# Kernel optimization log

Hardware: AMD Instinct MI355X
Metric: run time of the kernel (lower is better)

## Reference

```python
import jax, jax.numpy as jnp
import numpy as np
import math

B, C, T0, Q0 = 2, 48, 250, 65
H = 192; KS = 4; HS = 1; NH = 4; E = 8; F = 65; DV = 12; HID2 = 384
EPS = 1e-5


def ln_clamp(x, g, b, axes, eps=EPS):
    # LayerNormalization4D / 4DCF: std = sqrt(clamp(var, eps))
    mu = x.mean(axis=axes, keepdims=True)
    var = x.var(axis=axes, keepdims=True)
    return (x - mu) / jnp.sqrt(jnp.maximum(var, eps)) * g + b


def torch_ln(x, g, b, eps=EPS):
    # torch.nn.LayerNorm over last dim: sqrt(var + eps)
    mu = x.mean(axis=-1, keepdims=True)
    var = x.var(axis=-1, keepdims=True)
    return (x - mu) / jnp.sqrt(var + eps) * g + b


def mha(x, in_w, in_b, out_w, out_b, nh):
    # torch.nn.MultiheadAttention, batch_first, self-attention
    N, L, Cm = x.shape
    qkv = x @ in_w.T + in_b
    q, k, v = jnp.split(qkv, 3, axis=-1)
    dh = Cm // nh
    hd = lambda t: t.reshape(N, L, nh, dh).transpose(0, 2, 1, 3)
    q, k, v = hd(q), hd(k), hd(v)
    att = jax.nn.softmax(jnp.einsum('nhld,nhmd->nhlm', q, k) / jnp.sqrt(jnp.float32(dh)), axis=-1)
    o = jnp.einsum('nhlm,nhmd->nhld', att, v).transpose(0, 2, 1, 3).reshape(N, L, Cm)
    return o @ out_w.T + out_b


def lstm_dir(x, wi, wh, bi, bh, reverse=False):
    # x: [N, L, D]; torch gate order i,f,g,o
    Hd = wh.shape[1]
    xs = jnp.swapaxes(x, 0, 1)
    if reverse:
        xs = xs[::-1]
    pre = jnp.einsum('lnd,gd->lng', xs, wi) + bi + bh  # [L,N,4H]

    def step(carry, p):
        hprev, cprev = carry
        gates = p + hprev @ wh.T
        i, f, g, o = jnp.split(gates, 4, axis=-1)
        c = jax.nn.sigmoid(f) * cprev + jax.nn.sigmoid(i) * jnp.tanh(g)
        hnew = jax.nn.sigmoid(o) * jnp.tanh(c)
        return (hnew, c), hnew

    h0 = jnp.zeros((x.shape[0], Hd), x.dtype)
    _, ys = jax.lax.scan(step, (h0, h0), pre)
    if reverse:
        ys = ys[::-1]
    return jnp.swapaxes(ys, 0, 1)


def bilstm(x, wif, whf, bif, bhf, wib, whb, bib, bhb):
    return jnp.concatenate([lstm_dir(x, wif, whf, bif, bhf, False),
                            lstm_dir(x, wib, whb, bib, bhb, True)], axis=-1)


def unfold1d(x, ks, hs):
    # x: [N, C, Q] -> [N, L, C*ks], channel-major like F.unfold
    N, Cc, Qq = x.shape
    L = (Qq - ks) // hs + 1
    cols = jnp.stack([x[:, :, k:k + (L - 1) * hs + 1:hs] for k in range(ks)], axis=-1)  # [N,C,L,ks]
    return cols.transpose(0, 2, 1, 3).reshape(N, L, Cc * ks)


def conv_transpose1d(x, w, b, stride):
    # x: [N, Cin, L], w: [Cin, Cout, ks] (torch ConvTranspose1d layout); overlap-add
    N, Ci, L = x.shape
    ks = w.shape[2]
    out_len = (L - 1) * stride + ks
    y = jnp.einsum('nil,iok->nolk', x, w)
    out = jnp.zeros((N, w.shape[1], out_len), x.dtype)
    for k in range(ks):
        out = out.at[:, :, k:k + (L - 1) * stride + 1:stride].add(y[..., k])
    return out + b[:, None]


def _forward(x, af_in_w, af_in_b, af_out_w, af_out_b, naf_g, naf_b, at_in_w, at_in_b, at_out_w, at_out_b, nat_g, nat_b, intra_ng, intra_nb, inter_ng, inter_nb, intra_wif, intra_whf, intra_bif, intra_bhf, intra_wib, intra_whb, intra_bib, intra_bhb, inter_wif, inter_whf, inter_bif, inter_bhf, inter_wib, inter_whb, inter_bib, inter_bhb, il_w, il_b, itl_w, itl_b, qw, qb, qa, qg, qbt, kw, kb, ka, kg, kbt, vw, vb, va, vg, vbt, pw, pb, pa, pg, pbt, fin_w, fin_b, fdw_w, fdw_b, fout_w, fout_b):
    Bb, Cc, old_T, old_Q = x.shape
    T = math.ceil((old_T - KS) / HS) * HS + KS
    Qd = math.ceil((old_Q - KS) / HS) * HS + KS
    x = jnp.pad(x, ((0, 0), (0, 0), (0, T - old_T), (0, Qd - old_Q)))
    input_ = x

    # ---- intra (frequency) path ----
    z = ln_clamp(input_, intra_ng[None, :, None, None], intra_nb[None, :, None, None], (1,))
    seq = z.transpose(0, 2, 3, 1).reshape(Bb * T, Qd, Cc)  # [B*T, Q, C]
    att = mha(seq, af_in_w, af_in_b, af_out_w, af_out_b, NH)
    seq = torch_ln(att + seq, naf_g, naf_b)
    u = unfold1d(seq.transpose(0, 2, 1), KS, HS)
    r = bilstm(u, intra_wif, intra_whf, intra_bif, intra_bhf, intra_wib, intra_whb, intra_bib, intra_bhb)
    r = conv_transpose1d(r.transpose(0, 2, 1), il_w, il_b, HS)  # [B*T, C, Qd]
    intra = r.reshape(Bb, T, Cc, Qd).transpose(0, 2, 1, 3) + input_
    input_ = intra

    # ---- inter (time) path ----
    z = ln_clamp(input_, inter_ng[None, :, None, None], inter_nb[None, :, None, None], (1,))
    seq = z.transpose(0, 3, 2, 1).reshape(Bb * Qd, T, Cc)  # [B*Q, T, C]
    att = mha(seq, at_in_w, at_in_b, at_out_w, at_out_b, NH)
    seq = torch_ln(att + seq, nat_g, nat_b)
    u = unfold1d(seq.transpose(0, 2, 1), KS, HS)
    r = bilstm(u, inter_wif, inter_whf, inter_bif, inter_bhf, inter_wib, inter_whb, inter_bib, inter_bhb)
    r = conv_transpose1d(r.transpose(0, 2, 1), itl_w, itl_b, HS)  # [B*Qd, C, T]
    inter = r.reshape(Bb, Qd, Cc, T).transpose(0, 2, 3, 1) + input_
    inter = inter[:, :, :old_T, :old_Q]

    # ---- custom per-head conv attention ----
    bt = inter  # [B, C, t, f]

    def head_proj(w, bias, a, g, beta):
        y = jnp.einsum('bctf,hec->hbetf', bt, w) + bias[:, None, :, None, None]
        y = jnp.where(y >= 0, y, a[:, None, None, None, None] * y)  # PReLU per head
        return ln_clamp(y, g[:, None, :, None, :], beta[:, None, :, None, :], (2, 4))

    Qh = head_proj(qw, qb, qa, qg, qbt)  # [h,B,E,t,f]
    Kh = head_proj(kw, kb, ka, kg, kbt)
    Vh = head_proj(vw, vb, va, vg, vbt)  # [h,B,dv,t,f]
    h_, _, E_, t_, f_ = Qh.shape
    dv = Vh.shape[2]
    Qf = Qh.transpose(0, 1, 3, 2, 4).reshape(h_, Bb, t_, E_ * f_)
    Kf = Kh.transpose(0, 1, 3, 2, 4).reshape(h_, Bb, t_, E_ * f_)
    Vf = Vh.transpose(0, 1, 3, 2, 4).reshape(h_, Bb, t_, dv * f_)
    attm = jax.nn.softmax(jnp.einsum('hbtd,hbsd->hbts', Qf, Kf) / jnp.sqrt(jnp.float32(E_ * f_)), axis=-1)
    Vo = jnp.einsum('hbts,hbsd->hbtd', attm, Vf).reshape(h_, Bb, t_, dv, f_)
    Vo = Vo.transpose(1, 0, 3, 2, 4).reshape(Bb, h_ * dv, t_, f_)  # head-major channel concat
    pj = jnp.einsum('bctf,oc->botf', Vo, pw) + pb[None, :, None, None]
    pj = jnp.where(pj >= 0, pj, pa * pj)
    pj = ln_clamp(pj, pg[None, :, None, :], pbt[None, :, None, :], (1, 3))
    out = pj + inter

    # ---- gated-dconv FFN ----
    pi = jnp.einsum('bctf,oc->botf', out, fin_w) + fin_b[None, :, None, None]
    dwc = jax.lax.conv_general_dilated(pi, fdw_w, (1, 1), ((1, 1), (1, 1)),
                                       dimension_numbers=('NCHW', 'OIHW', 'NCHW'),
                                       feature_group_count=fdw_w.shape[0]) + fdw_b[None, :, None, None]
    x1, x2 = jnp.split(dwc, 2, axis=1)
    ffn = jnp.einsum('bctf,oc->botf', jax.nn.gelu(x1, approximate=False) * x2, fout_w) + fout_b[None, :, None, None]
    return ffn + out


def setup_inputs() -> dict:
    key = jax.random.key(0)
    cnt = [0]

    def rn(shape, s=0.05):
        cnt[0] += 1
        return jax.random.normal(jax.random.fold_in(key, cnt[0]), shape, dtype=jnp.float32) * s

    z = lambda *s: jnp.zeros(s, jnp.float32)
    o = lambda *s: jnp.ones(s, jnp.float32)
    d = {}
    d['x'] = rn((B, C, T0, Q0), 1.0)
    for p in ['af', 'at']:
        d[p + '_in_w'] = rn((3 * C, C)); d[p + '_in_b'] = z(3 * C)
        d[p + '_out_w'] = rn((C, C)); d[p + '_out_b'] = z(C)
    d['naf_g'] = o(C); d['naf_b'] = z(C); d['nat_g'] = o(C); d['nat_b'] = z(C)
    d['intra_ng'] = o(C); d['intra_nb'] = z(C); d['inter_ng'] = o(C); d['inter_nb'] = z(C)
    for p in ['intra', 'inter']:
        for s in ['f', 'b']:
            d[p + '_wi' + s] = rn((4 * H, C * KS)); d[p + '_wh' + s] = rn((4 * H, H))
            d[p + '_bi' + s] = z(4 * H); d[p + '_bh' + s] = z(4 * H)
    d['il_w'] = rn((2 * H, C, KS)); d['il_b'] = z(C)
    d['itl_w'] = rn((2 * H, C, KS)); d['itl_b'] = z(C)
    for p, dim in [('q', E), ('k', E), ('v', DV)]:
        d[p + 'w'] = rn((NH, dim, C)); d[p + 'b'] = z(NH, dim)
        d[p + 'a'] = 0.25 * o(NH); d[p + 'g'] = o(NH, dim, F); d[p + 'bt'] = z(NH, dim, F)
    d['pw'] = rn((C, C)); d['pb'] = z(C); d['pa'] = 0.25 * o(1); d['pg'] = o(C, F); d['pbt'] = z(C, F)
    d['fin_w'] = rn((HID2, C)); d['fin_b'] = z(HID2)
    d['fdw_w'] = rn((HID2, 1, 3, 3)); d['fdw_b'] = z(HID2)
    d['fout_w'] = rn((C, HID2 // 2)); d['fout_b'] = z(C)
    return d


def reference(x, af_in_w, af_in_b, af_out_w, af_out_b, naf_g, naf_b, at_in_w, at_in_b, at_out_w, at_out_b, nat_g, nat_b, intra_ng, intra_nb, inter_ng, inter_nb, intra_wif, intra_whf, intra_bif, intra_bhf, intra_wib, intra_whb, intra_bib, intra_bhb, inter_wif, inter_whf, inter_bif, inter_bhf, inter_wib, inter_whb, inter_bib, inter_bhb, il_w, il_b, itl_w, itl_b, qw, qb, qa, qg, qbt, kw, kb, ka, kg, kbt, vw, vb, va, vg, vbt, pw, pb, pa, pg, pbt, fin_w, fin_b, fdw_w, fdw_b, fout_w, fout_b):
    return _forward(x, af_in_w, af_in_b, af_out_w, af_out_b, naf_g, naf_b, at_in_w, at_in_b, at_out_w, at_out_b, nat_g, nat_b, intra_ng, intra_nb, inter_ng, inter_nb, intra_wif, intra_whf, intra_bif, intra_bhf, intra_wib, intra_whb, intra_bib, intra_bhb, inter_wif, inter_whf, inter_bif, inter_bhf, inter_wib, inter_whb, inter_bib, inter_bhb, il_w, il_b, itl_w, itl_b, qw, qb, qa, qg, qbt, kw, kb, ka, kg, kbt, vw, vb, va, vg, vbt, pw, pb, pa, pg, pbt, fin_w, fin_b, fdw_w, fdw_b, fout_w, fout_b)
```

## Files before the change

kernel.cpp:

```cpp
#include <hip/hip_runtime.h>
#include <math.h>

#define EPSV 1e-5f

typedef _Float16 v2h __attribute__((ext_vector_type(2)));

__device__ __forceinline__ float sigf(float x){ return 1.0f/(1.0f+__expf(-x)); }
__device__ __forceinline__ float tanhf_(float x){
  float c = fminf(fmaxf(x,-10.f),10.f);
  float e = __expf(2.0f*c);
  return (e-1.0f)/(e+1.0f);
}

__device__ __forceinline__ void ldsbar(){
  asm volatile("s_waitcnt lgkmcnt(0)\n\ts_barrier" ::: "memory");
}

__device__ __forceinline__ float dot2u(unsigned int a, unsigned int b, float c){
#if __has_builtin(__builtin_amdgcn_fdot2)
  v2h av = __builtin_bit_cast(v2h, a);
  v2h bv = __builtin_bit_cast(v2h, b);
  return __builtin_amdgcn_fdot2(av, bv, c, false);
#else
  v2h av = __builtin_bit_cast(v2h, a);
  v2h bv = __builtin_bit_cast(v2h, b);
  return c + (float)av.x*(float)bv.x + (float)av.y*(float)bv.y;
#endif
}

__global__ void k_ln_chan(const float* __restrict__ src, float* __restrict__ dst,
                          const float* __restrict__ g, const float* __restrict__ bb, int mode){
  int i = blockIdx.x*blockDim.x + threadIdx.x;
  const int total = 2*250*65;
  if (i >= total) return;
  int q = i % 65; int t = (i/65) % 250; int b = i/(65*250);
  const float* p = src + (size_t)b*48*250*65 + (size_t)t*65 + q;
  float s=0.f, ss=0.f;
  for (int c=0;c<48;c++){ float v = p[(size_t)c*250*65]; s+=v; ss+=v*v; }
  float mu = s*(1.0f/48.0f);
  float var = ss*(1.0f/48.0f) - mu*mu;
  float rs = rsqrtf(fmaxf(var, EPSV));
  float* d = (mode==0) ? dst + ((size_t)(b*250+t)*65 + q)*48
                       : dst + ((size_t)(b*65+q)*250 + t)*48;
  for (int c=0;c<48;c++){ float v = p[(size_t)c*250*65]; d[c] = (v-mu)*rs*g[c] + bb[c]; }
}

__global__ void k_qkv(const float* __restrict__ seq, const float* __restrict__ w,
                      const float* __restrict__ bias, float* __restrict__ qkv, int NL){
  int i = blockIdx.x*blockDim.x + threadIdx.x;
  if (i >= NL*144) return;
  int j = i % 144; int nl = i / 144;
  const float* srow = seq + (size_t)nl*48;
  const float* wrow = w + j*48;
  float acc = bias[j];
  for (int c=0;c<48;c++) acc += srow[c]*wrow[c];
  qkv[i] = acc;
}

__global__ void k_mha(const float* __restrict__ qkv, float* __restrict__ att, int N, int L){
  __shared__ float shq[250*12];
  __shared__ float shk[250*12];
  __shared__ float shv[250*12];
  int n = blockIdx.x, h = blockIdx.y;
  const float* base = qkv + (size_t)n*L*144 + h*12;
  for (int i = threadIdx.x; i < L*12; i += blockDim.x){
    int l = i/12, d = i%12;
    shq[i] = base[(size_t)l*144 + d];
    shk[i] = base[(size_t)l*144 + 48 + d];
    shv[i] = base[(size_t)l*144 + 96 + d];
  }
  __syncthreads();
  const float scale = 0.28867513459481287f;
  for (int r = threadIdx.x; r < L; r += blockDim.x){
    float m = -1e30f, den = 0.0f, o[12];
    for (int d=0; d<12; d++) o[d]=0.0f;
    const float* qr = shq + r*12;
    for (int j=0; j<L; j++){
      const float* kr = shk + j*12;
      float s = 0.f;
      for (int d=0; d<12; d++) s += qr[d]*kr[d];
      s *= scale;
      if (s > m){
        float corr = __expf(m - s);
        den *= corr;
        for (int d=0; d<12; d++) o[d] *= corr;
        m = s;
      }
      float e = __expf(s - m);
      den += e;
      const float* vr = shv + j*12;
      for (int d=0; d<12; d++) o[d] += e*vr[d];
    }
    float inv = 1.0f/den;
    float* outp = att + ((size_t)n*L + r)*48 + h*12;
    for (int d=0; d<12; d++) outp[d] = o[d]*inv;
  }
}

__global__ void k_projres(const float* __restrict__ att, const float* __restrict__ seq,
                          const float* __restrict__ w, const float* __restrict__ bias,
                          float* __restrict__ dst, int NL){
  int i = blockIdx.x*blockDim.x + threadIdx.x;
  if (i >= NL*48) return;
  int o = i % 48; int nl = i/48;
  const float* ar = att + (size_t)nl*48;
  const float* wr = w + o*48;
  float acc = bias[o] + seq[i];
  for (int c=0;c<48;c++) acc += ar[c]*wr[c];
  dst[i] = acc;
}

__global__ void k_rowln(float* __restrict__ buf, const float* __restrict__ g,
                        const float* __restrict__ bb, int NL){
  int nl = blockIdx.x*blockDim.x + threadIdx.x;
  if (nl >= NL) return;
  float* p = buf + (size_t)nl*48;
  float s=0.f, ss=0.f;
  for (int c=0;c<48;c++){ float v=p[c]; s+=v; ss+=v*v; }
  float mu = s*(1.0f/48.0f);
  float var = ss*(1.0f/48.0f) - mu*mu;
  float rs = rsqrtf(var + EPSV);
  for (int c=0;c<48;c++) p[c] = (p[c]-mu)*rs*g[c] + bb[c];
}

__global__ void k_prep(const float* __restrict__ s0, const float* __restrict__ s1,
                       const float* __restrict__ s2, const float* __restrict__ s3,
                       const float* __restrict__ s4, const float* __restrict__ s5,
                       const float* __restrict__ s6, const float* __restrict__ s7,
                       const float* __restrict__ c0, const float* __restrict__ c1,
                       unsigned int* __restrict__ wpk, unsigned int* __restrict__ wtp){
  int i = blockIdx.x*blockDim.x + threadIdx.x;
  if (i < 589824){
    int seg = i/73728, off = i - seg*73728;
    const float* w = (seg==0)?s0:(seg==1)?s1:(seg==2)?s2:(seg==3)?s3:(seg==4)?s4:(seg==5)?s5:(seg==6)?s6:s7;
    int g = off % 768, d2 = off / 768;
    v2h v; v.x = (_Float16)w[g*192 + 2*d2]; v.y = (_Float16)w[g*192 + 2*d2 + 1];
    wpk[(size_t)seg*73728 + (size_t)d2*768 + g] = __builtin_bit_cast(unsigned int, v);
  } else if (i < 589824 + 2*36864){
    int j = i - 589824;
    int seg = j/36864, off = j - seg*36864;
    const float* w = seg ? c1 : c0;
    int c = off % 48; int ii2 = (off/48) % 192; int k = off/(48*192);
    v2h v;
    v.x = (_Float16)w[(2*ii2)*192 + c*4 + k];
    v.y = (_Float16)w[(2*ii2+1)*192 + c*4 + k];
    wtp[(size_t)seg*36864 + off] = __builtin_bit_cast(unsigned int, v);
  }
}

__global__ __launch_bounds__(256) void k_pregates(
    const float* __restrict__ seq2, const unsigned int* __restrict__ wi,
    const float* __restrict__ bi, const float* __restrict__ bh,
    _Float16* __restrict__ pre, int L2, int SL){
  __shared__ unsigned int ut[96*16];
  int n = blockIdx.y;
  int l0 = blockIdx.x*16;
  int t = threadIdx.x;
  for (int idx=t; idx<1536; idx+=256){
    int l = idx & 15, d2 = idx >> 4;
    int li = l0 + l;
    int c = d2 >> 1, k0 = (d2 & 1)*2;
    float u0=0.f, u1=0.f;
    if (li < L2){
      const float* p = seq2 + ((size_t)n*SL + li)*48;
      u0 = p[k0*48 + c];
      u1 = p[(k0+1)*48 + c];
    }
    v2h v; v.x=(_Float16)u0; v.y=(_Float16)u1;
    ut[d2*16 + l] = __builtin_bit_cast(unsigned int, v);
  }
  __syncthreads();
  float acc[3][16];
  float b0 = bi[t] + bh[t];
  float b1 = bi[t+256] + bh[t+256];
  float b2 = bi[t+512] + bh[t+512];
  #pragma unroll
  for (int l=0;l<16;l++){ acc[0][l]=b0; acc[1][l]=b1; acc[2][l]=b2; }
  #pragma unroll 4
  for (int d2=0; d2<96; d2++){
    unsigned int w0 = wi[(size_t)d2*768 + t];
    unsigned int w1 = wi[(size_t)d2*768 + t + 256];
    unsigned int w2 = wi[(size_t)d2*768 + t + 512];
    const uint4* u4 = (const uint4*)(ut + d2*16);
    #pragma unroll
    for (int l4=0; l4<4; l4++){
      uint4 uu = u4[l4];
      acc[0][l4*4+0] = dot2u(uu.x, w0, acc[0][l4*4+0]);
      acc[0][l4*4+1] = dot2u(uu.y, w0, acc[0][l4*4+1]);
      acc[0][l4*4+2] = dot2u(uu.z, w0, acc[0][l4*4+2]);
      acc[0][l4*4+3] = dot2u(uu.w, w0, acc[0][l4*4+3]);
      acc[1][l4*4+0] = dot2u(uu.x, w1, acc[1][l4*4+0]);
      acc[1][l4*4+1] = dot2u(uu.y, w1, acc[1][l4*4+1]);
      acc[1][l4*4+2] = dot2u(uu.z, w1, acc[1][l4*4+2]);
      acc[1][l4*4+3] = dot2u(uu.w, w1, acc[1][l4*4+3]);
      acc[2][l4*4+0] = dot2u(uu.x, w2, acc[2][l4*4+0]);
      acc[2][l4*4+1] = dot2u(uu.y, w2, acc[2][l4*4+1]);
      acc[2][l4*4+2] = dot2u(uu.z, w2, acc[2][l4*4+2]);
      acc[2][l4*4+3] = dot2u(uu.w, w2, acc[2][l4*4+3]);
    }
  }
  #pragma unroll
  for (int l=0;l<16;l++){
    int li = l0 + l;
    if (li < L2){
      _Float16* pr = pre + ((size_t)n*L2 + li)*768;
      pr[t]       = (_Float16)acc[0][l];
      pr[t+256]   = (_Float16)acc[1][l];
      pr[t+512]   = (_Float16)acc[2][l];
    }
  }
}

template<int G>
__global__ __launch_bounds__(1024) void k_lstm6(
    const _Float16* __restrict__ pre, unsigned int* __restrict__ rT2,
    const unsigned int* __restrict__ wh_f, const unsigned int* __restrict__ wh_b,
    int N, int L2){
  __shared__ unsigned int hh2[96*G];
  __shared__ float gpart[4*G*768];
  _Float16* hh2h = (_Float16*)hh2;
  int t = threadIdx.x;
  int q = t >> 8, tt = t & 255;
  int dir = blockIdx.y;
  int n0 = blockIdx.x*G;
  const unsigned int* wh = dir ? wh_b : wh_f;
  unsigned int wq[24][3];
  #pragma unroll
  for (int i=0;i<24;i++){
    const unsigned int* wr = wh + (size_t)(q*24+i)*768 + tt;
    wq[i][0] = wr[0]; wq[i][1] = wr[256]; wq[i][2] = wr[512];
  }
  const _Float16* prd = pre + (size_t)dir*(size_t)N*L2*768;
  float cst = 0.f;
  int as = t/192, aj = t - as*192;
  bool actv = (t < 192*G);
  const unsigned short* pbase = (const unsigned short*)prd;
  if (actv) pbase = (const unsigned short*)(prd + ((size_t)(n0+as)*L2)*768) + aj;
  for (int idx=t; idx<96*G; idx+=1024) hh2[idx]=0u;
  __syncthreads();

  unsigned short c0=0,c1=0,c2=0,c3=0;
  {
    int l0 = dir ? (L2-1) : 0;
    if (actv){
      const unsigned short* pp = pbase + (size_t)l0*768;
      c0 = pp[0]; c1 = pp[192]; c2 = pp[384]; c3 = pp[576];
    }
  }

  for (int step=0; step<L2; step++){
    int l = dir ? (L2-1-step) : step;
    int stepn = (step+1 < L2) ? (step+1) : step;
    int ln = dir ? (L2-1-stepn) : stepn;
    unsigned short pn0=0,pn1=0,pn2=0,pn3=0;
    if (actv){
      const unsigned short* pp = pbase + (size_t)ln*768;
      pn0 = pp[0]; pn1 = pp[192]; pn2 = pp[384]; pn3 = pp[576];
    }

    float acc0[G], acc1[G], acc2[G];
    #pragma unroll
    for (int s=0;s<G;s++){ acc0[s]=0.f; acc1[s]=0.f; acc2[s]=0.f; }
    #pragma unroll
    for (int i=0;i<24;i++){
      unsigned int hhv[G];
      if (G==4){
        uint4 hv = ((const uint4*)hh2)[q*24+i];
        hhv[0]=hv.x; hhv[1]=hv.y; hhv[2]=hv.z; hhv[3]=hv.w;
      } else if (G==2){
        uint2 hv = ((const uint2*)hh2)[q*24+i];
        hhv[0]=hv.x; hhv[1]=hv.y;
      } else {
        hhv[0] = hh2[q*24+i];
      }
      unsigned int w0 = wq[i][0], w1 = wq[i][1], w2 = wq[i][2];
      #pragma unroll
      for (int s=0;s<G;s++){
        acc0[s] = dot2u(hhv[s], w0, acc0[s]);
        acc1[s] = dot2u(hhv[s], w1, acc1[s]);
        acc2[s] = dot2u(hhv[s], w2, acc2[s]);
      }
    }
    #pragma unroll
    for (int s=0;s<G;s++){
      gpart[(q*G+s)*768 + tt]       = acc0[s];
      gpart[(q*G+s)*768 + tt + 256] = acc1[s];
      gpart[(q*G+s)*768 + tt + 512] = acc2[s];
    }
    ldsbar();

    if (actv){
      float gi = (float)__builtin_bit_cast(_Float16, c0);
      float gf = (float)__builtin_bit_cast(_Float16, c1);
      float gg = (float)__builtin_bit_cast(_Float16, c2);
      float go = (float)__builtin_bit_cast(_Float16, c3);
      #pragma unroll
      for (int qq=0; qq<4; qq++){
        const float* gp = gpart + (qq*G+as)*768;
        gi += gp[aj]; gf += gp[aj+192]; gg += gp[aj+384]; go += gp[aj+576];
      }
      float ig = sigf(gi), fg = sigf(gf), g2 = tanhf_(gg), og = sigf(go);
      cst = fg*cst + ig*g2;
      float hn = og*tanhf_(cst);
      hh2h[((aj>>1)*G + as)*2 + (aj&1)] = (_Float16)hn;
    }
    ldsbar();

    if (t < 96*G){
      int s = t/96, ii2 = t - s*96;
      unsigned int v = hh2[ii2*G + s];
      rT2[((size_t)(n0+s)*192 + dir*96 + ii2)*L2 + l] = v;
    }
    c0 = pn0; c1 = pn1; c2 = pn2; c3 = pn3;
  }
}

__global__ __launch_bounds__(256) void k_convt4(
    const unsigned int* __restrict__ rT2, const unsigned int* __restrict__ wtp,
    const float* __restrict__ bias, const float* __restrict__ resid,
    float* __restrict__ dst, int L2, int OL, int mode){
  int n = blockIdx.y;
  int pos = blockIdx.x*64 + (threadIdx.x & 63);
  int cq = __builtin_amdgcn_readfirstlane((int)(threadIdx.x >> 6));
  float acc[12];
  #pragma unroll
  for (int c=0;c<12;c++) acc[c]=0.f;
  const unsigned int* rbase = rT2 + (size_t)n*192*L2;
  for (int k=0;k<4;k++){
    int l = pos - k;
    bool v = (l>=0) && (l<L2);
    int lc = v ? l : 0;
    const unsigned int* wk = wtp + (size_t)k*192*48 + cq*12;
    #pragma unroll 4
    for (int ii2=0; ii2<192; ii2++){
      unsigned int rp = v ? rbase[(size_t)ii2*L2 + lc] : 0u;
      const unsigned int* wrow = wk + ii2*48;
      #pragma unroll
      for (int c=0;c<12;c++) acc[c] = dot2u(rp, wrow[c], acc[c]);
    }
  }
  if (pos < OL){
    for (int c12=0;c12<12;c12++){
      int c = cq*12 + c12;
      size_t oidx;
      if (mode==0){ int b=n/250, t=n%250; oidx = (((size_t)b*48+c)*250+t)*65+pos; }
      else        { int b=n/65,  qq=n%65; oidx = (((size_t)b*48+c)*250+pos)*65+qq; }
      dst[oidx] = acc[c12] + bias[c] + resid[oidx];
    }
  }
}

__global__ __launch_bounds__(256) void k_hproj(
    const float* __restrict__ bt, const float* __restrict__ w,
    const float* __restrict__ bias, const float* __restrict__ alpha,
    const float* __restrict__ g, const float* __restrict__ beta,
    float* __restrict__ dst, int dim, int kt_mode){
  __shared__ float ybuf[780];
  __shared__ float r1[256];
  __shared__ float r2[256];
  int bx = blockIdx.x;
  int h = bx/500; int rem = bx - h*500; int b = rem/250; int t = rem - b*250;
  int ny = dim*65;
  int tid = threadIdx.x;
  const float* bbase = bt + (size_t)b*48*250*65 + (size_t)t*65;
  float al = alpha[h];
  float s=0.f, ss=0.f;
  for (int kidx=tid; kidx<ny; kidx+=256){
    int e = kidx/65, f = kidx - e*65;
    const float* wr = w + (h*dim+e)*48;
    float acc = bias[h*dim+e];
    for (int c=0;c<48;c++) acc += bbase[(size_t)c*250*65 + f]*wr[c];
    if (acc < 0.f) acc *= al;
    ybuf[kidx] = acc; s += acc; ss += acc*acc;
  }
  r1[tid]=s; r2[tid]=ss; __syncthreads();
  for (int st=128; st>0; st>>=1){
    if (tid<st){ r1[tid]+=r1[tid+st]; r2[tid]+=r2[tid+st]; }
    __syncthreads();
  }
  float mu = r1[0]/(float)ny, var = r2[0]/(float)ny - mu*mu;
  float rs = rsqrtf(fmaxf(var, EPSV));
  for (int kidx=tid; kidx<ny; kidx+=256){
    float y = (ybuf[kidx]-mu)*rs*g[h*ny+kidx] + beta[h*ny+kidx];
    if (kt_mode) dst[((size_t)(h*2+b)*520 + kidx)*250 + t] = y;
    else         dst[(size_t)bx*ny + kidx] = y;
  }
}

__global__ __launch_bounds__(256) void k_headattn2(
    const float* __restrict__ Qp, const float* __restrict__ KT,
    const float* __restrict__ Vp, float* __restrict__ Vo){
  __shared__ float qsh[10*520];
  __shared__ float psh[10*250];
  __shared__ float rinv[10];
  int t0 = blockIdx.x*10;
  int hb = blockIdx.y;
  int h = hb >> 1, b = hb & 1;
  int tid = threadIdx.x;
  const float* qbase = Qp + ((size_t)hb*250 + t0)*520;
  for (int i=tid; i<5200; i+=256) qsh[i] = qbase[i];
  __syncthreads();
  const float scale = 0.04385290096535147f;
  if (tid < 250){
    float sc[10];
    #pragma unroll
    for (int i=0;i<10;i++) sc[i]=0.f;
    const float* kcol = KT + (size_t)hb*520*250 + tid;
    for (int d=0; d<520; d++){
      float kv = kcol[(size_t)d*250];
      #pragma unroll
      for (int i=0;i<10;i++) sc[i] += qsh[i*520+d]*kv;
    }
    #pragma unroll
    for (int i=0;i<10;i++) psh[i*250+tid] = sc[i]*scale;
  }
  __syncthreads();
  if (tid < 10){
    float m = -1e30f;
    for (int s2=0;s2<250;s2++) m = fmaxf(m, psh[tid*250+s2]);
    float den = 0.f;
    for (int s2=0;s2<250;s2++){
      float e = __expf(psh[tid*250+s2]-m);
      psh[tid*250+s2]=e; den+=e;
    }
    rinv[tid] = 1.0f/den;
  }
  __syncthreads();
  float acc[10][4];
  #pragma unroll
  for (int i=0;i<10;i++)
    #pragma unroll
    for (int s=0;s<4;s++) acc[i][s]=0.f;
  for (int s2=0; s2<250; s2++){
    const float* vrow = Vp + ((size_t)hb*250 + s2)*780;
    float p[10];
    #pragma unroll
    for (int i=0;i<10;i++) p[i] = psh[i*250+s2];
    #pragma unroll
    for (int slot=0; slot<4; slot++){
      int d = tid + slot*256;
      if (d < 780){
        float v = vrow[d];
        #pragma unroll
        for (int i=0;i<10;i++) acc[i][slot] += p[i]*v;
      }
    }
  }
  #pragma unroll
  for (int slot=0; slot<4; slot++){
    int d = tid + slot*256;
    if (d < 780){
      int e = d/65, f = d - e*65;
      #pragma unroll
      for (int i=0;i<10;i++){
        Vo[(((size_t)b*48 + h*12 + e)*250 + (t0+i))*65 + f] = acc[i][slot]*rinv[i];
      }
    }
  }
}

__global__ void k_pproj(const float* __restrict__ Vo, const float* __restrict__ pw,
                        const float* __restrict__ pb, const float* __restrict__ pa,
                        float* __restrict__ pj){
  int i = blockIdx.x*blockDim.x + threadIdx.x;
  if (i >= 2*48*250*65) return;
  int f = i % 65;
  int t = (i/65) % 250;
  int o = (i/(65*250)) % 48;
  int b = i/(65*250*48);
  const float* vp = Vo + (size_t)b*48*250*65 + (size_t)t*65 + f;
  const float* wr = pw + o*48;
  float acc = pb[o];
  for (int c=0;c<48;c++) acc += vp[(size_t)c*250*65]*wr[c];
  if (acc < 0.f) acc *= pa[0];
  pj[i] = acc;
}

__global__ void k_pln(const float* __restrict__ pj, const float* __restrict__ pg,
                      const float* __restrict__ pbt, const float* __restrict__ inter,
                      float* __restrict__ outb){
  __shared__ float r1[256];
  __shared__ float r2[256];
  int bx = blockIdx.x;
  int t = bx % 250, b = bx/250;
  const float* base = pj + (size_t)b*48*250*65 + (size_t)t*65;
  float s=0.f, ss=0.f;
  for (int k=threadIdx.x; k<3120; k+=256){
    int c = k/65, f = k%65;
    float v = base[(size_t)c*250*65 + f];
    s+=v; ss+=v*v;
  }
  r1[threadIdx.x]=s; r2[threadIdx.x]=ss; __syncthreads();
  for (int st=128; st>0; st>>=1){
    if (threadIdx.x<st){ r1[threadIdx.x]+=r1[threadIdx.x+st]; r2[threadIdx.x]+=r2[threadIdx.x+st]; }
    __syncthreads();
  }
  float mu = r1[0]*(1.0f/3120.0f), var = r2[0]*(1.0f/3120.0f) - mu*mu;
  float rs = rsqrtf(fmaxf(var, EPSV));
  for (int k=threadIdx.x; k<3120; k+=256){
    int c = k/65, f = k%65;
    size_t idx = (((size_t)b*48+c)*250 + t)*65 + f;
    float v = pj[idx];
    outb[idx] = (v-mu)*rs*pg[c*65+f] + pbt[c*65+f] + inter[idx];
  }
}

__global__ void k_fin2(const float* __restrict__ outb, const float* __restrict__ w,
                       const float* __restrict__ bias, float* __restrict__ pi){
  int i = blockIdx.x*blockDim.x + threadIdx.x;
  if (i >= 2*96*250*65) return;
  int f = i % 65;
  int t = (i/65) % 250;
  int og = (i/(65*250)) % 96;
  int b = i/(65*250*96);
  const float* xp = outb + (size_t)b*48*250*65 + (size_t)t*65 + f;
  const float* w0 = w + og*4*48;
  float a0=bias[og*4], a1=bias[og*4+1], a2=bias[og*4+2], a3=bias[og*4+3];
  for (int c=0;c<48;c++){
    float xv = xp[(size_t)c*250*65];
    a0 += xv*w0[c]; a1 += xv*w0[48+c]; a2 += xv*w0[96+c]; a3 += xv*w0[144+c];
  }
  size_t o0 = (((size_t)b*384 + og*4)*250 + t)*65 + f;
  pi[o0] = a0; pi[o0+16250] = a1; pi[o0+2*16250] = a2; pi[o0+3*16250] = a3;
}

__global__ void k_dwg(const float* __restrict__ pi, const float* __restrict__ dw,
                      const float* __restrict__ db, float* __restrict__ gbuf){
  int i = blockIdx.x*blockDim.x + threadIdx.x;
  if (i >= 2*192*250*65) return;
  int f = i % 65;
  int t = (i/65) % 250;
  int j = (i/(65*250)) % 192;
  int b = i/(65*250*192);
  float x12[2];
  for (int half=0; half<2; half++){
    int ch = j + half*192;
    const float* base = pi + ((size_t)b*384 + ch)*250*65;
    const float* wr = dw + ch*9;
    float acc = db[ch];
    for (int dt=-1; dt<=1; dt++){
      int tt = t+dt;
      if (tt<0||tt>=250) continue;
      for (int df=-1; df<=1; df++){
        int ff = f+df;
        if (ff<0||ff>=65) continue;
        acc += base[(size_t)tt*65+ff]*wr[(dt+1)*3 + (df+1)];
      }
    }
    x12[half]=acc;
  }
  float x1 = x12[0];
  float g = 0.5f*x1*(1.0f+erff(x1*0.70710678118654752f));
  gbuf[i] = g * x12[1];
}

__global__ void k_final2(const float* __restrict__ gbuf, const float* __restrict__ w,
                         const float* __restrict__ bias, const float* __restrict__ outb,
                         float* __restrict__ dout){
  int i = blockIdx.x*blockDim.x + threadIdx.x;
  if (i >= 2*12*250*65) return;
  int f = i % 65;
  int t = (i/65) % 250;
  int og = (i/(65*250)) % 12;
  int b = i/(65*250*12);
  const float* gp = gbuf + (size_t)b*192*250*65 + (size_t)t*65 + f;
  const float* w0 = w + og*4*192;
  float a0=bias[og*4], a1=bias[og*4+1], a2=bias[og*4+2], a3=bias[og*4+3];
  for (int j=0;j<192;j++){
    float gv = gp[(size_t)j*250*65];
    a0 += gv*w0[j]; a1 += gv*w0[192+j]; a2 += gv*w0[384+j]; a3 += gv*w0[576+j];
  }
  size_t o0 = (((size_t)b*48 + og*4)*250 + t)*65 + f;
  dout[o0]         = a0 + outb[o0];
  dout[o0+16250]   = a1 + outb[o0+16250];
  dout[o0+2*16250] = a2 + outb[o0+2*16250];
  dout[o0+3*16250] = a3 + outb[o0+3*16250];
}

extern "C" void kernel_launch(void* const* d_in, const int* in_sizes, int n_in,
                              void* d_out, int out_size, void* d_ws, size_t ws_size,
                              hipStream_t stream) {
  (void)in_sizes; (void)n_in; (void)out_size; (void)ws_size;
  auto in = [&](int i){ return (const float*)d_in[i]; };
  const float* x        = in(0);
  const float* af_in_w  = in(1);  const float* af_in_b  = in(2);
  const float* af_out_w = in(3);  const float* af_out_b = in(4);
  const float* at_in_w  = in(5);  const float* at_in_b  = in(6);
  const float* at_out_w = in(7);  const float* at_out_b = in(8);
  const float* naf_g = in(9),  *naf_b = in(10), *nat_g = in(11), *nat_b = in(12);
  const float* intra_ng = in(13), *intra_nb = in(14), *inter_ng = in(15), *inter_nb = in(16);
  const float* intra_wif = in(17), *intra_whf = in(18), *intra_bif = in(19), *intra_bhf = in(20);
  const float* intra_wib = in(21), *intra_whb = in(22), *intra_bib = in(23), *intra_bhb = in(24);
  const float* inter_wif = in(25), *inter_whf = in(26), *inter_bif = in(27), *inter_bhf = in(28);
  const float* inter_wib = in(29), *inter_whb = in(30), *inter_bib = in(31), *inter_bhb = in(32);
  const float* il_w = in(33), *il_b = in(34), *itl_w = in(35), *itl_b = in(36);
  const float* qw = in(37), *qb = in(38), *qa = in(39), *qg = in(40), *qbt = in(41);
  const float* kw = in(42), *kb = in(43), *ka = in(44), *kg = in(45), *kbt = in(46);
  const float* vw = in(47), *vb = in(48), *va = in(49), *vg = in(50), *vbt = in(51);
  const float* pw = in(52), *pb = in(53), *pa = in(54), *pg = in(55), *pbt = in(56);
  const float* fin_w = in(57), *fin_b = in(58), *fdw_w = in(59), *fdw_b = in(60);
  const float* fout_w = in(61), *fout_b = in(62);

  float* ws = (float*)d_ws;
  float* buf_intra = ws + 0;
  float* buf_bt    = ws + 1560000;
  float* buf_out   = ws + 3120000;
  unsigned int* wpk = (unsigned int*)(ws + 4680000);
  unsigned int* wtp = (unsigned int*)(ws + 5269824);
  float* scr       = ws + 5343552;
  float* s_seq2 = scr;
  float* s_seq  = scr + 1560000;
  float* s_qkv  = scr + 3120000;
  float* s_att  = scr + 7800000;
  _Float16* s_pre = (_Float16*)(scr + 1560000);
  unsigned int* s_rT2 = (unsigned int*)(scr + 26220480);
  float* s_Qh = scr;
  float* s_KT = scr + 1040000;
  float* s_Vh = scr + 2080000;
  float* s_Vo = scr + 3640000;
  float* s_pj = scr + 5200000;
  float* s_pi = scr;
  float* s_g  = scr + 12480000;

  const int thr = 256;
  auto cdiv = [](int a, int b){ return (a+b-1)/b; };

  k_prep<<<cdiv(663552,thr),thr,0,stream>>>(
      intra_wif, intra_whf, intra_wib, intra_whb,
      inter_wif, inter_whf, inter_wib, inter_whb,
      il_w, itl_w, wpk, wtp);

  k_ln_chan<<<cdiv(2*250*65,thr), thr, 0, stream>>>(x, s_seq, intra_ng, intra_nb, 0);
  k_qkv<<<cdiv(500*65*144,thr), thr, 0, stream>>>(s_seq, af_in_w, af_in_b, s_qkv, 500*65);
  k_mha<<<dim3(500,4), 256, 0, stream>>>(s_qkv, s_att, 500, 65);
  k_projres<<<cdiv(500*65*48,thr), thr, 0, stream>>>(s_att, s_seq, af_out_w, af_out_b, s_seq2, 500*65);
  k_rowln<<<cdiv(32500,thr), thr, 0, stream>>>(s_seq2, naf_g, naf_b, 32500);
  {
    const size_t dstr = (size_t)500*62*768;
    k_pregates<<<dim3(4,500), 256, 0, stream>>>(s_seq2, wpk+0*73728, intra_bif, intra_bhf, s_pre,        62, 65);
    k_pregates<<<dim3(4,500), 256, 0, stream>>>(s_seq2, wpk+2*73728, intra_bib, intra_bhb, s_pre + dstr, 62, 65);
  }
  k_lstm6<2><<<dim3(250,2), 1024, 0, stream>>>(s_pre, s_rT2, wpk+1*73728, wpk+3*73728, 500, 62);
  k_convt4<<<dim3(2,500), 256, 0, stream>>>(s_rT2, wtp+0*36864, il_b, x, buf_intra, 62, 65, 0);

  k_ln_chan<<<cdiv(2*250*65,thr),thr,0,stream>>>(buf_intra, s_seq, inter_ng, inter_nb, 1);
  k_qkv<<<cdiv(130*250*144,thr),thr,0,stream>>>(s_seq, at_in_w, at_in_b, s_qkv, 130*250);
  k_mha<<<dim3(130,4), 256, 0, stream>>>(s_qkv, s_att, 130, 250);
  k_projres<<<cdiv(130*250*48,thr),thr,0,stream>>>(s_att, s_seq, at_out_w, at_out_b, s_seq2, 130*250);
  k_rowln<<<cdiv(32500,thr),thr,0,stream>>>(s_seq2, nat_g, nat_b, 32500);
  {
    const size_t dstr = (size_t)130*247*768;
    k_pregates<<<dim3(16,130), 256, 0, stream>>>(s_seq2, wpk+4*73728, inter_bif, inter_bhf, s_pre,        247, 250);
    k_pregates<<<dim3(16,130), 256, 0, stream>>>(s_seq2, wpk+6*73728, inter_bib, inter_bhb, s_pre + dstr, 247, 250);
  }
  k_lstm6<1><<<dim3(130,2), 1024, 0, stream>>>(s_pre, s_rT2, wpk+5*73728, wpk+7*73728, 130, 247);
  k_convt4<<<dim3(4,130), 256, 0, stream>>>(s_rT2, wtp+1*36864, itl_b, buf_intra, buf_bt, 247, 250, 1);

  k_hproj<<<2000,256,0,stream>>>(buf_bt, qw, qb, qa, qg, qbt, s_Qh, 8, 0);
  k_hproj<<<2000,256,0,stream>>>(buf_bt, kw, kb, ka, kg, kbt, s_KT, 8, 1);
  k_hproj<<<2000,256,0,stream>>>(buf_bt, vw, vb, va, vg, vbt, s_Vh, 12, 0);
  k_headattn2<<<dim3(25,8), 256, 0, stream>>>(s_Qh, s_KT, s_Vh, s_Vo);
  k_pproj<<<cdiv(2*48*250*65,thr),thr,0,stream>>>(s_Vo, pw, pb, pa, s_pj);
  k_pln<<<500,256,0,stream>>>(s_pj, pg, pbt, buf_bt, buf_out);

  k_fin2<<<cdiv(2*96*250*65,thr),thr,0,stream>>>(buf_out, fin_w, fin_b, s_pi);
  k_dwg<<<cdiv(2*192*250*65,thr),thr,0,stream>>>(s_pi, fdw_w, fdw_b, s_g);
  k_final2<<<cdiv(2*12*250*65,thr),thr,0,stream>>>(s_g, fout_w, fout_b, buf_out, (float*)d_out);
}
```

Measured before the change: 2.577 ms.

## Fuse QKV projection into MHA and P-projection into its layernorm kernel

The separate QKV linear kernel is folded into the attention kernel, which now computes each head's Q/K/V directly into shared memory. The attention inner loop is rewritten with float4 shared-memory loads. The P projection and its layernorm/residual are merged into one per-(b,t) block that stages Vo in shared memory, and the hproj kernel stages its input slice in shared memory too. This removes the large qkv and pj intermediate buffers and several launches, at the cost of recomputing nothing but with more serialized per-block work in the projection phase.

```diff
diff --git a/kernel.cpp b/kernel.cpp
--- a/kernel.cpp
+++ b/kernel.cpp
@@ -45,55 +45,59 @@
   for (int c=0;c<48;c++){ float v = p[(size_t)c*250*65]; d[c] = (v-mu)*rs*g[c] + bb[c]; }
 }
 
-__global__ void k_qkv(const float* __restrict__ seq, const float* __restrict__ w,
-                      const float* __restrict__ bias, float* __restrict__ qkv, int NL){
-  int i = blockIdx.x*blockDim.x + threadIdx.x;
-  if (i >= NL*144) return;
-  int j = i % 144; int nl = i / 144;
-  const float* srow = seq + (size_t)nl*48;
-  const float* wrow = w + j*48;
-  float acc = bias[j];
-  for (int c=0;c<48;c++) acc += srow[c]*wrow[c];
-  qkv[i] = acc;
-}
-
-__global__ void k_mha(const float* __restrict__ qkv, float* __restrict__ att, int N, int L){
+__global__ __launch_bounds__(256) void k_mha2(
+    const float* __restrict__ seq, const float* __restrict__ inw,
+    const float* __restrict__ inb, float* __restrict__ att, int N, int L){
   __shared__ float shq[250*12];
   __shared__ float shk[250*12];
   __shared__ float shv[250*12];
   int n = blockIdx.x, h = blockIdx.y;
-  const float* base = qkv + (size_t)n*L*144 + h*12;
-  for (int i = threadIdx.x; i < L*12; i += blockDim.x){
-    int l = i/12, d = i%12;
-    shq[i] = base[(size_t)l*144 + d];
-    shk[i] = base[(size_t)l*144 + 48 + d];
-    shv[i] = base[(size_t)l*144 + 96 + d];
+  for (int i = threadIdx.x; i < L*36; i += 256){
+    int l = i/36, jj = i - (i/36)*36;
+    int sect = jj/12, d = jj - sect*12;
+    int j = sect*48 + h*12 + d;
+    const float* srow = seq + ((size_t)n*L + l)*48;
+    const float* wrow = inw + j*48;
+    float acc = inb[j];
+    for (int c=0;c<48;c++) acc += srow[c]*wrow[c];
+    float* dst = (sect==0)?shq:(sect==1)?shk:shv;
+    dst[l*12+d] = acc;
   }
   __syncthreads();
   const float scale = 0.28867513459481287f;
-  for (int r = threadIdx.x; r < L; r += blockDim.x){
-    float m = -1e30f, den = 0.0f, o[12];
-    for (int d=0; d<12; d++) o[d]=0.0f;
-    const float* qr = shq + r*12;
+  for (int r = threadIdx.x; r < L; r += 256){
+    const float4* q4 = (const float4*)(shq + r*12);
+    float4 q0 = q4[0], q1 = q4[1], q2 = q4[2];
+    float m = -1e30f, den = 0.0f;
+    float4 o0 = make_float4(0,0,0,0), o1 = make_float4(0,0,0,0), o2 = make_float4(0,0,0,0);
     for (int j=0; j<L; j++){
-      const float* kr = shk + j*12;
-      float s = 0.f;
-      for (int d=0; d<12; d++) s += qr[d]*kr[d];
+      const float4* k4 = (const float4*)(shk + j*12);
+      float4 k0 = k4[0], k1 = k4[1], k2 = k4[2];
+      float s = q0.x*k0.x + q0.y*k0.y + q0.z*k0.z + q0.w*k0.w
+              + q1.x*k1.x + q1.y*k1.y + q1.z*k1.z + q1.w*k1.w
+              + q2.x*k2.x + q2.y*k2.y + q2.z*k2.z + q2.w*k2.w;
       s *= scale;
       if (s > m){
         float corr = __expf(m - s);
         den *= corr;
-        for (int d=0; d<12; d++) o[d] *= corr;
+        o0.x*=corr; o0.y*=corr; o0.z*=corr; o0.w*=corr;
+        o1.x*=corr; o1.y*=corr; o1.z*=corr; o1.w*=corr;
+        o2.x*=corr; o2.y*=corr; o2.z*=corr; o2.w*=corr;
         m = s;
       }
       float e = __expf(s - m);
       den += e;
-      const float* vr = shv + j*12;
-      for (int d=0; d<12; d++) o[d] += e*vr[d];
+      const float4* v4 = (const float4*)(shv + j*12);
+      float4 v0 = v4[0], v1 = v4[1], v2 = v4[2];
+      o0.x += e*v0.x; o0.y += e*v0.y; o0.z += e*v0.z; o0.w += e*v0.w;
+      o1.x += e*v1.x; o1.y += e*v1.y; o1.z += e*v1.z; o1.w += e*v1.w;
+      o2.x += e*v2.x; o2.y += e*v2.y; o2.z += e*v2.z; o2.w += e*v2.w;
     }
     float inv = 1.0f/den;
     float* outp = att + ((size_t)n*L + r)*48 + h*12;
-    for (int d=0; d<12; d++) outp[d] = o[d]*inv;
+    outp[0]=o0.x*inv; outp[1]=o0.y*inv; outp[2]=o0.z*inv; outp[3]=o0.w*inv;
+    outp[4]=o1.x*inv; outp[5]=o1.y*inv; outp[6]=o1.z*inv; outp[7]=o1.w*inv;
+    outp[8]=o2.x*inv; outp[9]=o2.y*inv; outp[10]=o2.z*inv; outp[11]=o2.w*inv;
   }
 }
 
@@ -355,6 +359,7 @@
     const float* __restrict__ bias, const float* __restrict__ alpha,
     const float* __restrict__ g, const float* __restrict__ beta,
     float* __restrict__ dst, int dim, int kt_mode){
+  __shared__ float tsh[3120];
   __shared__ float ybuf[780];
   __shared__ float r1[256];
   __shared__ float r2[256];
@@ -363,13 +368,18 @@
   int ny = dim*65;
   int tid = threadIdx.x;
   const float* bbase = bt + (size_t)b*48*250*65 + (size_t)t*65;
+  for (int kidx=tid; kidx<3120; kidx+=256){
+    int c = kidx/65, f = kidx - c*65;
+    tsh[kidx] = bbase[(size_t)c*250*65 + f];
+  }
+  __syncthreads();
   float al = alpha[h];
   float s=0.f, ss=0.f;
   for (int kidx=tid; kidx<ny; kidx+=256){
     int e = kidx/65, f = kidx - e*65;
     const float* wr = w + (h*dim+e)*48;
     float acc = bias[h*dim+e];
-    for (int c=0;c<48;c++) acc += bbase[(size_t)c*250*65 + f]*wr[c];
+    for (int c=0;c<48;c++) acc += tsh[c*65+f]*wr[c];
     if (acc < 0.f) acc *= al;
     ybuf[kidx] = acc; s += acc; ss += acc*acc;
   }
@@ -459,49 +469,45 @@
   }
 }
 
-__global__ void k_pproj(const float* __restrict__ Vo, const float* __restrict__ pw,
-                        const float* __restrict__ pb, const float* __restrict__ pa,
-                        float* __restrict__ pj){
-  int i = blockIdx.x*blockDim.x + threadIdx.x;
-  if (i >= 2*48*250*65) return;
-  int f = i % 65;
-  int t = (i/65) % 250;
-  int o = (i/(65*250)) % 48;
-  int b = i/(65*250*48);
-  const float* vp = Vo + (size_t)b*48*250*65 + (size_t)t*65 + f;
-  const float* wr = pw + o*48;
-  float acc = pb[o];
-  for (int c=0;c<48;c++) acc += vp[(size_t)c*250*65]*wr[c];
-  if (acc < 0.f) acc *= pa[0];
-  pj[i] = acc;
-}
-
-__global__ void k_pln(const float* __restrict__ pj, const float* __restrict__ pg,
-                      const float* __restrict__ pbt, const float* __restrict__ inter,
-                      float* __restrict__ outb){
+__global__ __launch_bounds__(256) void k_pprojln(
+    const float* __restrict__ Vo, const float* __restrict__ pw,
+    const float* __restrict__ pb, const float* __restrict__ pa,
+    const float* __restrict__ pg, const float* __restrict__ pbt,
+    const float* __restrict__ inter, float* __restrict__ outb){
+  __shared__ float vsh[3120];
+  __shared__ float ysh[3120];
   __shared__ float r1[256];
   __shared__ float r2[256];
   int bx = blockIdx.x;
   int t = bx % 250, b = bx/250;
-  const float* base = pj + (size_t)b*48*250*65 + (size_t)t*65;
+  int tid = threadIdx.x;
+  const float* vbase = Vo + (size_t)b*48*250*65 + (size_t)t*65;
+  for (int k=tid; k<3120; k+=256){
+    int c = k/65, f = k - c*65;
+    vsh[k] = vbase[(size_t)c*250*65 + f];
+  }
+  __syncthreads();
+  float pav = pa[0];
   float s=0.f, ss=0.f;
-  for (int k=threadIdx.x; k<3120; k+=256){
-    int c = k/65, f = k%65;
-    float v = base[(size_t)c*250*65 + f];
-    s+=v; ss+=v*v;
-  }
-  r1[threadIdx.x]=s; r2[threadIdx.x]=ss; __syncthreads();
+  for (int k=tid; k<3120; k+=256){
+    int o = k/65, f = k - o*65;
+    const float* wr = pw + o*48;
+    float acc = pb[o];
+    for (int c=0;c<48;c++) acc += vsh[c*65+f]*wr[c];
+    if (acc < 0.f) acc *= pav;
+    ysh[k] = acc; s += acc; ss += acc*acc;
+  }
+  r1[tid]=s; r2[tid]=ss; __syncthreads();
   for (int st=128; st>0; st>>=1){
-    if (threadIdx.x<st){ r1[threadIdx.x]+=r1[threadIdx.x+st]; r2[threadIdx.x]+=r2[threadIdx.x+st]; }
+    if (tid<st){ r1[tid]+=r1[tid+st]; r2[tid]+=r2[tid+st]; }
     __syncthreads();
   }
   float mu = r1[0]*(1.0f/3120.0f), var = r2[0]*(1.0f/3120.0f) - mu*mu;
   float rs = rsqrtf(fmaxf(var, EPSV));
-  for (int k=threadIdx.x; k<3120; k+=256){
-    int c = k/65, f = k%65;
+  for (int k=tid; k<3120; k+=256){
+    int c = k/65, f = k - c*65;
     size_t idx = (((size_t)b*48+c)*250 + t)*65 + f;
-    float v = pj[idx];
-    outb[idx] = (v-mu)*rs*pg[c*65+f] + pbt[c*65+f] + inter[idx];
+    outb[idx] = (ysh[k]-mu)*rs*pg[k] + pbt[k] + inter[idx];
   }
 }
 
@@ -610,15 +616,13 @@
   float* scr       = ws + 5343552;
   float* s_seq2 = scr;
   float* s_seq  = scr + 1560000;
-  float* s_qkv  = scr + 3120000;
-  float* s_att  = scr + 7800000;
-  _Float16* s_pre = (_Float16*)(scr + 1560000);
-  unsigned int* s_rT2 = (unsigned int*)(scr + 26220480);
+  float* s_att  = scr + 3120000;
+  _Float16* s_pre = (_Float16*)(scr + 4680000);
+  unsigned int* s_rT2 = (unsigned int*)(scr + 29340480);
   float* s_Qh = scr;
   float* s_KT = scr + 1040000;
   float* s_Vh = scr + 2080000;
   float* s_Vo = scr + 3640000;
-  float* s_pj = scr + 5200000;
   float* s_pi = scr;
   float* s_g  = scr + 12480000;
 
@@ -631,8 +635,7 @@
       il_w, itl_w, wpk, wtp);
 
   k_ln_chan<<<cdiv(2*250*65,thr), thr, 0, stream>>>(x, s_seq, intra_ng, intra_nb, 0);
-  k_qkv<<<cdiv(500*65*144,thr), thr, 0, stream>>>(s_seq, af_in_w, af_in_b, s_qkv, 500*65);
-  k_mha<<<dim3(500,4), 256, 0, stream>>>(s_qkv, s_att, 500, 65);
+  k_mha2<<<dim3(500,4), 256, 0, stream>>>(s_seq, af_in_w, af_in_b, s_att, 500, 65);
   k_projres<<<cdiv(500*65*48,thr), thr, 0, stream>>>(s_att, s_seq, af_out_w, af_out_b, s_seq2, 500*65);
   k_rowln<<<cdiv(32500,thr), thr, 0, stream>>>(s_seq2, naf_g, naf_b, 32500);
   {
@@ -644,8 +647,7 @@
   k_convt4<<<dim3(2,500), 256, 0, stream>>>(s_rT2, wtp+0*36864, il_b, x, buf_intra, 62, 65, 0);
 
   k_ln_chan<<<cdiv(2*250*65,thr),thr,0,stream>>>(buf_intra, s_seq, inter_ng, inter_nb, 1);
-  k_qkv<<<cdiv(130*250*144,thr),thr,0,stream>>>(s_seq, at_in_w, at_in_b, s_qkv, 130*250);
-  k_mha<<<dim3(130,4), 256, 0, stream>>>(s_qkv, s_att, 130, 250);
+  k_mha2<<<dim3(130,4), 256, 0, stream>>>(s_seq, at_in_w, at_in_b, s_att, 130, 250);
   k_projres<<<cdiv(130*250*48,thr),thr,0,stream>>>(s_att, s_seq, at_out_w, at_out_b, s_seq2, 130*250);
   k_rowln<<<cdiv(32500,thr),thr,0,stream>>>(s_seq2, nat_g, nat_b, 32500);
   {
@@ -660,8 +662,7 @@
   k_hproj<<<2000,256,0,stream>>>(buf_bt, kw, kb, ka, kg, kbt, s_KT, 8, 1);
   k_hproj<<<2000,256,0,stream>>>(buf_bt, vw, vb, va, vg, vbt, s_Vh, 12, 0);
   k_headattn2<<<dim3(25,8), 256, 0, stream>>>(s_Qh, s_KT, s_Vh, s_Vo);
-  k_pproj<<<cdiv(2*48*250*65,thr),thr,0,stream>>>(s_Vo, pw, pb, pa, s_pj);
-  k_pln<<<500,256,0,stream>>>(s_pj, pg, pbt, buf_bt, buf_out);
+  k_pprojln<<<500,256,0,stream>>>(s_Vo, pw, pb, pa, pg, pbt, buf_bt, buf_out);
 
   k_fin2<<<cdiv(2*96*250*65,thr),thr,0,stream>>>(buf_out, fin_w, fin_b, s_pi);
   k_dwg<<<cdiv(2*192*250*65,thr),thr,0,stream>>>(s_pi, fdw_w, fdw_b, s_g);
```

Measured after the change: 2.542 ms. About the same (-1.4%).
